# Kernel optimization log

Hardware: AMD Instinct MI355X
Metric: run time of the kernel (lower is better)

The kernel has to match this reference:

```python
import jax, jax.numpy as jnp
import numpy as np

N_NODES = 100000
N_EDGES = 3200000
N_FEAT = 128
HIDDEN = 16


def gcn_conv(x, W, b, row, col, ew, n):
    """PyG GCNConv: linear -> add self-loops -> sym deg-norm -> scatter-add -> bias."""
    x = x @ W  # [n, out]
    loop = jnp.arange(n)
    row = jnp.concatenate([row, loop])
    col = jnp.concatenate([col, loop])
    ew = jnp.concatenate([ew, jnp.ones((n,), ew.dtype)])  # self-loop weight 1
    deg = jax.ops.segment_sum(ew, col, num_segments=n)  # in-degree by edge weight
    dinv = jnp.where(deg > 0, jax.lax.rsqrt(deg), 0.0)
    norm = dinv[row] * ew * dinv[col]  # [E+n]
    # gather source features, scale, scatter-add at destinations
    out = jax.ops.segment_sum(x[row] * norm[:, None], col, num_segments=n)
    return out + b


def setup_inputs() -> dict:
    key = jax.random.key(0)
    k = jax.random.split(key, 7)
    x = jax.random.normal(k[0], (N_NODES, N_FEAT), dtype=jnp.float32)
    edge_index = jax.random.randint(k[1], (2, N_EDGES), 0, N_NODES, dtype=jnp.int64)
    edge_weight = jax.random.uniform(k[2], (N_EDGES,), dtype=jnp.float32)
    s1 = 1.0 / np.sqrt(N_FEAT)
    s2 = 1.0 / np.sqrt(HIDDEN)
    W1 = jax.random.uniform(k[3], (N_FEAT, HIDDEN), jnp.float32, -s1, s1)
    b1 = jnp.zeros((HIDDEN,), jnp.float32)
    W2 = jax.random.uniform(k[4], (HIDDEN, 1), jnp.float32, -s2, s2)
    b2 = jnp.zeros((1,), jnp.float32)
    return {"x": x, "edge_index": edge_index, "edge_weight": edge_weight,
            "W1": W1, "b1": b1, "W2": W2, "b2": b2}


def reference(x, edge_index, edge_weight, W1, b1, W2, b2):
    n = x.shape[0]
    row, col = edge_index[0], edge_index[1]
    h = gcn_conv(x, W1, b1, row, col, edge_weight, n)
    h = jax.nn.relu(h)
    h = gcn_conv(h, W2, b2, row, col, edge_weight, n)
    return jax.nn.sigmoid(h)[:, 0].astype(jnp.float32)  # squeeze(1)
```

## Files before the change

### kernel.cpp

```cpp
#include <hip/hip_runtime.h>
#include <hip/hip_fp16.h>
#include <math.h>

#define NNODES 100000
#define NEDGES 3200000
#define NF 128
#define NH 16
#define SB 192
#define NSB 521
#define NBLK 512
#define EPB (NEDGES / NBLK)
#define CAP2 6912
#define XWBLK 391

__device__ __forceinline__ __half2 u2h(unsigned u) { union { unsigned u; __half2 h; } c; c.u = u; return c.h; }
__device__ __forceinline__ unsigned h2u(__half2 h) { union { unsigned u; __half2 h; } c; c.h = h; return c.u; }
__device__ __forceinline__ __half2 shfl_h2(__half2 v, int m) {
    int x = __shfl_xor(*(int*)&v, m);
    return *(__half2*)&x;
}

__global__ void k_histxw(const int* __restrict__ col, unsigned* __restrict__ ghist,
                         const float* __restrict__ x, const float* __restrict__ W1,
                         float* __restrict__ xw) {
    __shared__ float w[NF * NH];
    __shared__ unsigned h[NSB];
    int t = threadIdx.x, b = blockIdx.x;
    if (b < NBLK) {
        for (int i = t; i < NSB; i += 256) h[i] = 0u;
        __syncthreads();
        const int2* c2 = (const int2*)(col + b * EPB);
        for (int i = t; i < EPB / 2; i += 256) {
            int2 c = c2[i];
            atomicAdd(&h[(unsigned)c.x / SB], 1u);
            atomicAdd(&h[(unsigned)c.y / SB], 1u);
        }
        __syncthreads();
        for (int i = t; i < NSB; i += 256) ghist[(size_t)b * NSB + i] = h[i];
    } else {
        for (int i = t; i < NF * NH; i += 256) w[i] = W1[i];
        __syncthreads();
        int i = (b - NBLK) * 256 + t;
        if (i >= NNODES) return;
        float acc[NH];
#pragma unroll
        for (int f = 0; f < NH; ++f) acc[f] = 0.f;
        const float4* xr = (const float4*)(x + (long long)i * NF);
#pragma unroll 8
        for (int k4 = 0; k4 < NF / 4; ++k4) {
            float4 v = xr[k4];
            const float* wk = &w[k4 * 4 * NH];
#pragma unroll
            for (int f = 0; f < NH; ++f)
                acc[f] += v.x * wk[f] + v.y * wk[NH + f] + v.z * wk[2 * NH + f] + v.w * wk[3 * NH + f];
        }
        float4* o = (float4*)(xw + (size_t)i * NH);
#pragma unroll
        for (int q = 0; q < 4; ++q)
            o[q] = make_float4(acc[4 * q], acc[4 * q + 1], acc[4 * q + 2], acc[4 * q + 3]);
    }
}

__global__ __launch_bounds__(NBLK) void k_scan1(unsigned* __restrict__ ghist,
                                                unsigned* __restrict__ totals) {
    int k = blockIdx.x, t = threadIdx.x;
    __shared__ unsigned s[NBLK];
    unsigned v = ghist[(size_t)t * NSB + k];
    s[t] = v;
    __syncthreads();
    for (int off = 1; off < NBLK; off <<= 1) {
        unsigned x = (t >= off) ? s[t - off] : 0u;
        __syncthreads();
        s[t] += x;
        __syncthreads();
    }
    ghist[(size_t)t * NSB + k] = s[t] - v;
    if (t == NBLK - 1) totals[k] = s[t];
}

__global__ void k_scan2(const unsigned* __restrict__ totals, unsigned* __restrict__ sbase,
                        unsigned* __restrict__ start) {
    int t = threadIdx.x;
    __shared__ unsigned s[256];
    unsigned v[3];
    unsigned p = 0;
#pragma unroll
    for (int j = 0; j < 3; ++j) {
        int i = t * 3 + j;
        v[j] = (i < NSB) ? totals[i] : 0u;
        p += v[j];
    }
    s[t] = p;
    __syncthreads();
    for (int off = 1; off < 256; off <<= 1) {
        unsigned x = (t >= off) ? s[t - off] : 0u;
        __syncthreads();
        s[t] += x;
        __syncthreads();
    }
    unsigned run = s[t] - p;
#pragma unroll
    for (int j = 0; j < 3; ++j) {
        int i = t * 3 + j;
        if (i < NSB) sbase[i] = run;
        run += v[j];
    }
    if (t == 255) { sbase[NSB] = NEDGES; start[NNODES] = NEDGES; }
}

__global__ __launch_bounds__(256) void k_scatB1(
        const int* __restrict__ row, const int* __restrict__ col,
        const float* __restrict__ ew,
        const unsigned* __restrict__ ghist, const unsigned* __restrict__ sbase,
        uint2* __restrict__ spack) {
    __shared__ uint2 stage[EPB];
    __shared__ unsigned short sbArr[EPB];
    __shared__ unsigned lcnt[NSB];
    __shared__ unsigned gdelta[NSB];
    __shared__ unsigned scn[256];
    int t = threadIdx.x, b = blockIdx.x;
    int e0 = b * EPB;
    for (int i = t; i < NSB; i += 256) lcnt[i] = 0u;
    __syncthreads();
    const int2* c2 = (const int2*)(col + e0);
    for (int i = t; i < EPB / 2; i += 256) {
        int2 c = c2[i];
        atomicAdd(&lcnt[(unsigned)c.x / SB], 1u);
        atomicAdd(&lcnt[(unsigned)c.y / SB], 1u);
    }
    __syncthreads();
    unsigned v[3];
    unsigned p = 0;
#pragma unroll
    for (int j = 0; j < 3; ++j) {
        int i = t * 3 + j;
        v[j] = (i < NSB) ? lcnt[i] : 0u;
        p += v[j];
    }
    scn[t] = p;
    __syncthreads();
    for (int off = 1; off < 256; off <<= 1) {
        unsigned x = (t >= off) ? scn[t - off] : 0u;
        __syncthreads();
        scn[t] += x;
        __syncthreads();
    }
    unsigned run = scn[t] - p;
    __syncthreads();
    unsigned lst[3];
#pragma unroll
    for (int j = 0; j < 3; ++j) {
        int i = t * 3 + j;
        if (i < NSB) {
            lst[j] = run;
            gdelta[i] = sbase[i] + ghist[(size_t)b * NSB + i] - run;
        }
        run += v[j];
    }
    __syncthreads();
#pragma unroll
    for (int j = 0; j < 3; ++j) {
        int i = t * 3 + j;
        if (i < NSB) lcnt[i] = lst[j];
    }
    __syncthreads();
    const int2* r2 = (const int2*)(row + e0);
    const float2* w2 = (const float2*)(ew + e0);
    for (int i = t; i < EPB / 2; i += 256) {
        int2 rr = r2[i];
        int2 cc = c2[i];
        float2 ww = w2[i];
        unsigned sb = (unsigned)cc.x / SB;
        unsigned ln = (unsigned)cc.x - sb * SB;
        unsigned pos = atomicAdd(&lcnt[sb], 1u);
        stage[pos] = make_uint2((unsigned)rr.x | (ln << 17), __float_as_uint(ww.x));
        sbArr[pos] = (unsigned short)sb;
        sb = (unsigned)cc.y / SB;
        ln = (unsigned)cc.y - sb * SB;
        pos = atomicAdd(&lcnt[sb], 1u);
        stage[pos] = make_uint2((unsigned)rr.y | (ln << 17), __float_as_uint(ww.y));
        sbArr[pos] = (unsigned short)sb;
    }
    __syncthreads();
    for (int i = t; i < EPB; i += 256)
        spack[i + gdelta[sbArr[i]]] = stage[i];
}

__global__ __launch_bounds__(512) void k_degdinv(
        const uint2* __restrict__ spack, const unsigned* __restrict__ sbase,
        unsigned* __restrict__ start, float* __restrict__ dinv,
        const float* __restrict__ xw, unsigned* __restrict__ xwn) {
    __shared__ unsigned hist[SB];
    __shared__ float wdeg[SB];
    __shared__ unsigned scn[512];
    int k = blockIdx.x, t = threadIdx.x;
    unsigned e0 = sbase[k], e1 = sbase[k + 1];
    int ne = (int)(e1 - e0);
    if (t < SB) { hist[t] = 0u; wdeg[t] = 0.f; }
    __syncthreads();
    for (int i = t; i < ne; i += 512) {
        uint2 p = spack[e0 + i];
        unsigned ln = p.x >> 17;
        atomicAdd(&hist[ln], 1u);
        atomicAdd(&wdeg[ln], __uint_as_float(p.y));
    }
    __syncthreads();
    unsigned v = (t < SB) ? hist[t] : 0u;
    scn[t] = v;
    __syncthreads();
    for (int off = 1; off < 512; off <<= 1) {
        unsigned x = (t >= off) ? scn[t - off] : 0u;
        __syncthreads();
        scn[t] += x;
        __syncthreads();
    }
    unsigned excl = scn[t] - v;
    int g = k * SB + t;
    if (t < SB && g < NNODES) {
        start[g] = e0 + excl;
        float di = rsqrtf(wdeg[t] + 1.0f);
        dinv[g] = di;
        const float4* xr = (const float4*)(xw + (size_t)g * NH);
        float4 A = xr[0], B = xr[1], C = xr[2], D = xr[3];
        uint4 o0, o1;
        o0.x = h2u(__floats2half2_rn(A.x * di, A.y * di));
        o0.y = h2u(__floats2half2_rn(A.z * di, A.w * di));
        o0.z = h2u(__floats2half2_rn(B.x * di, B.y * di));
        o0.w = h2u(__floats2half2_rn(B.z * di, B.w * di));
        o1.x = h2u(__floats2half2_rn(C.x * di, C.y * di));
        o1.y = h2u(__floats2half2_rn(C.z * di, C.w * di));
        o1.z = h2u(__floats2half2_rn(D.x * di, D.y * di));
        o1.w = h2u(__floats2half2_rn(D.z * di, D.w * di));
        uint4* o = (uint4*)(xwn + (size_t)g * 8);
        o[0] = o0;
        o[1] = o1;
    }
}

__global__ __launch_bounds__(1024) void k_sedge1(
        const uint2* __restrict__ spack, const unsigned* __restrict__ sbase,
        const unsigned* __restrict__ start, const unsigned* __restrict__ xwn,
        const float* __restrict__ dinv, const float* __restrict__ b1,
        const float* __restrict__ W2, float* __restrict__ zn) {
    __shared__ uint2 ed[CAP2];
    __shared__ unsigned lcnt[SB];
    int k = blockIdx.x, t = threadIdx.x;
    unsigned e0 = sbase[k], e1 = sbase[k + 1];
    int ne = (int)(e1 - e0);
    if (t < SB) {
        int g = k * SB + t;
        lcnt[t] = (g < NNODES) ? (start[g] - e0) : (unsigned)ne;
    }
    __syncthreads();
    for (int i = t; i < ne; i += 1024) {
        uint2 p = spack[e0 + i];
        unsigned ln = p.x >> 17;
        unsigned pos = atomicAdd(&lcnt[ln], 1u);
        __half2 hw = __float2half2_rn(__uint_as_float(p.y));
        ed[pos] = make_uint2(p.x & 0x1FFFFu, h2u(hw));
    }
    __syncthreads();
    int wave = t >> 6, lane = t & 63;
    int fg = lane & 3, e4 = lane >> 2;
#pragma unroll
    for (int j = 0; j < SB / 16; ++j) {
        int ln = wave * (SB / 16) + j;
        int g = k * SB + ln;
        if (g >= NNODES) break;
        unsigned o0 = (ln == 0) ? 0u : lcnt[ln - 1];
        unsigned o1 = lcnt[ln];
        __half2 a0 = __float2half2_rn(0.f), a1 = a0;
        for (unsigned e = o0 + e4; e < o1; e += 16) {
            uint2 d = ed[e];
            uint2 q = *(const uint2*)(xwn + (size_t)d.x * 8 + fg * 2);
            a0 = __hfma2(u2h(q.x), u2h(d.y), a0);
            a1 = __hfma2(u2h(q.y), u2h(d.y), a1);
        }
#pragma unroll
        for (int m = 4; m < 64; m <<= 1) {
            a0 = __hadd2(a0, shfl_h2(a0, m));
            a1 = __hadd2(a1, shfl_h2(a1, m));
        }
        float ax = __low2float(a0), ay = __high2float(a0);
        float az = __low2float(a1), aw = __high2float(a1);
        uint2 qs = *(const uint2*)(xwn + (size_t)g * 8 + fg * 2);
        ax += __low2float(u2h(qs.x)); ay += __high2float(u2h(qs.x));
        az += __low2float(u2h(qs.y)); aw += __high2float(u2h(qs.y));
        float di = dinv[g];
        float4 b4 = ((const float4*)b1)[fg];
        float4 w4 = ((const float4*)W2)[fg];
        float s = fmaxf(di * ax + b4.x, 0.f) * w4.x
                + fmaxf(di * ay + b4.y, 0.f) * w4.y
                + fmaxf(di * az + b4.z, 0.f) * w4.z
                + fmaxf(di * aw + b4.w, 0.f) * w4.w;
        s += __shfl_xor(s, 1);
        s += __shfl_xor(s, 2);
        if (lane == 0) zn[g] = s * di;
    }
}

__global__ __launch_bounds__(512) void k_edge2acc(
        const uint2* __restrict__ spack, const unsigned* __restrict__ sbase,
        const float* __restrict__ zn, const float* __restrict__ dinv,
        const float* __restrict__ b2, float* __restrict__ out) {
    __shared__ float zacc[SB];
    int k = blockIdx.x, t = threadIdx.x;
    if (t < SB) zacc[t] = 0.f;
    __syncthreads();
    unsigned e0 = sbase[k], e1 = sbase[k + 1];
    for (unsigned e = e0 + t; e < e1; e += 512) {
        uint2 p = spack[e];
        atomicAdd(&zacc[p.x >> 17], zn[p.x & 0x1FFFFu] * __uint_as_float(p.y));
    }
    __syncthreads();
    int g = k * SB + t;
    if (t < SB && g < NNODES) {
        float di = dinv[g];
        float v = di * zacc[t] + di * zn[g] + b2[0];
        out[g] = 1.f / (1.f + expf(-v));
    }
}

extern "C" void kernel_launch(void* const* d_in, const int* in_sizes, int n_in,
                              void* d_out, int out_size, void* d_ws, size_t ws_size,
                              hipStream_t stream) {
    const float* x  = (const float*)d_in[0];
    const int* eidx = (const int*)d_in[1];
    const float* ew = (const float*)d_in[2];
    const float* W1 = (const float*)d_in[3];
    const float* b1 = (const float*)d_in[4];
    const float* W2 = (const float*)d_in[5];
    const float* b2 = (const float*)d_in[6];
    float* out = (float*)d_out;

    const int* row = eidx;
    const int* col = eidx + NEDGES;

    unsigned* ws = (unsigned*)d_ws;
    uint2*    spack  = (uint2*)ws;
    float*    xw     = (float*)(ws + 6400000);
    unsigned* xwn    = ws + 8000000;
    float*    dinv   = (float*)(ws + 8800000);
    float*    zn     = (float*)(ws + 8900000);
    unsigned* start  = ws + 9000000;
    unsigned* sbase  = ws + 9100001;
    unsigned* totals = ws + 9100523;
    unsigned* ghist  = ws + 9101044;

    k_histxw <<<NBLK + XWBLK, 256, 0, stream>>>(col, ghist, x, W1, xw);
    k_scan1  <<<NSB, NBLK, 0, stream>>>(ghist, totals);
    k_scan2  <<<1, 256, 0, stream>>>(totals, sbase, start);
    k_scatB1 <<<NBLK, 256, 0, stream>>>(row, col, ew, ghist, sbase, spack);
    k_degdinv<<<NSB, 512, 0, stream>>>(spack, sbase, start, dinv, xw, xwn);
    k_sedge1 <<<NSB, 1024, 0, stream>>>(spack, sbase, start, xwn, dinv, b1, W2, zn);
    k_edge2acc<<<NSB, 512, 0, stream>>>(spack, sbase, zn, dinv, b2, out);
}
```

Measured before the change: 139.4 us.

## Fold superblock scan into scatter kernel and store XW in half precision

Removes the single-block k_scan2 launch by having every scatter block redundantly scan the superblock totals, with block 0 writing sbase. XW is now written directly as fp16 by the histogram/matmul kernel, and the source-side dinv scaling moves from a per-node prescale into the per-edge weight during edge staging. The scatter kernel also goes from 256 to 512 threads per block. This trades one launch and an XW fp32 round trip for a redundant scan per block and an extra dinv gather per edge, and it no longer writes start[NNODES].

```diff
diff --git a/kernel.cpp b/kernel.cpp
--- a/kernel.cpp
+++ b/kernel.cpp
@@ -22,7 +22,7 @@
 
 __global__ void k_histxw(const int* __restrict__ col, unsigned* __restrict__ ghist,
                          const float* __restrict__ x, const float* __restrict__ W1,
-                         float* __restrict__ xw) {
+                         unsigned* __restrict__ xwh) {
     __shared__ float w[NF * NH];
     __shared__ unsigned h[NSB];
     int t = threadIdx.x, b = blockIdx.x;
@@ -54,10 +54,13 @@
             for (int f = 0; f < NH; ++f)
                 acc[f] += v.x * wk[f] + v.y * wk[NH + f] + v.z * wk[2 * NH + f] + v.w * wk[3 * NH + f];
         }
-        float4* o = (float4*)(xw + (size_t)i * NH);
-#pragma unroll
-        for (int q = 0; q < 4; ++q)
-            o[q] = make_float4(acc[4 * q], acc[4 * q + 1], acc[4 * q + 2], acc[4 * q + 3]);
+        unsigned u[8];
+#pragma unroll
+        for (int j = 0; j < 8; ++j)
+            u[j] = h2u(__floats2half2_rn(acc[2 * j], acc[2 * j + 1]));
+        uint4* o = (uint4*)(xwh + (size_t)i * 8);
+        o[0] = make_uint4(u[0], u[1], u[2], u[3]);
+        o[1] = make_uint4(u[4], u[5], u[6], u[7]);
     }
 }
 
@@ -78,68 +81,59 @@
     if (t == NBLK - 1) totals[k] = s[t];
 }
 
-__global__ void k_scan2(const unsigned* __restrict__ totals, unsigned* __restrict__ sbase,
-                        unsigned* __restrict__ start) {
-    int t = threadIdx.x;
-    __shared__ unsigned s[256];
-    unsigned v[3];
-    unsigned p = 0;
-#pragma unroll
-    for (int j = 0; j < 3; ++j) {
-        int i = t * 3 + j;
-        v[j] = (i < NSB) ? totals[i] : 0u;
-        p += v[j];
-    }
-    s[t] = p;
-    __syncthreads();
-    for (int off = 1; off < 256; off <<= 1) {
-        unsigned x = (t >= off) ? s[t - off] : 0u;
-        __syncthreads();
-        s[t] += x;
-        __syncthreads();
-    }
-    unsigned run = s[t] - p;
-#pragma unroll
-    for (int j = 0; j < 3; ++j) {
-        int i = t * 3 + j;
-        if (i < NSB) sbase[i] = run;
-        run += v[j];
-    }
-    if (t == 255) { sbase[NSB] = NEDGES; start[NNODES] = NEDGES; }
-}
-
-__global__ __launch_bounds__(256) void k_scatB1(
+__global__ __launch_bounds__(512) void k_scatB1(
         const int* __restrict__ row, const int* __restrict__ col,
         const float* __restrict__ ew,
-        const unsigned* __restrict__ ghist, const unsigned* __restrict__ sbase,
-        uint2* __restrict__ spack) {
+        const unsigned* __restrict__ ghist, const unsigned* __restrict__ totals,
+        uint2* __restrict__ spack, unsigned* __restrict__ sbase_out) {
     __shared__ uint2 stage[EPB];
     __shared__ unsigned short sbArr[EPB];
     __shared__ unsigned lcnt[NSB];
     __shared__ unsigned gdelta[NSB];
-    __shared__ unsigned scn[256];
+    __shared__ unsigned scn[512];
     int t = threadIdx.x, b = blockIdx.x;
     int e0 = b * EPB;
-    for (int i = t; i < NSB; i += 256) lcnt[i] = 0u;
+    for (int i = t; i < NSB; i += 512) lcnt[i] = 0u;
     __syncthreads();
     const int2* c2 = (const int2*)(col + e0);
-    for (int i = t; i < EPB / 2; i += 256) {
+    for (int i = t; i < EPB / 2; i += 512) {
         int2 c = c2[i];
         atomicAdd(&lcnt[(unsigned)c.x / SB], 1u);
         atomicAdd(&lcnt[(unsigned)c.y / SB], 1u);
     }
     __syncthreads();
-    unsigned v[3];
+    unsigned tv[2];
+    unsigned tp = 0;
+#pragma unroll
+    for (int j = 0; j < 2; ++j) {
+        int i = t * 2 + j;
+        tv[j] = (i < NSB) ? totals[i] : 0u;
+        tp += tv[j];
+    }
+    scn[t] = tp;
+    __syncthreads();
+    for (int off = 1; off < 512; off <<= 1) {
+        unsigned x = (t >= off) ? scn[t - off] : 0u;
+        __syncthreads();
+        scn[t] += x;
+        __syncthreads();
+    }
+    unsigned trun = scn[t] - tp;
+    unsigned sb_[2];
+#pragma unroll
+    for (int j = 0; j < 2; ++j) { sb_[j] = trun; trun += tv[j]; }
+    __syncthreads();
+    unsigned v[2];
     unsigned p = 0;
 #pragma unroll
-    for (int j = 0; j < 3; ++j) {
-        int i = t * 3 + j;
+    for (int j = 0; j < 2; ++j) {
+        int i = t * 2 + j;
         v[j] = (i < NSB) ? lcnt[i] : 0u;
         p += v[j];
     }
     scn[t] = p;
     __syncthreads();
-    for (int off = 1; off < 256; off <<= 1) {
+    for (int off = 1; off < 512; off <<= 1) {
         unsigned x = (t >= off) ? scn[t - off] : 0u;
         __syncthreads();
         scn[t] += x;
@@ -147,26 +141,34 @@
     }
     unsigned run = scn[t] - p;
     __syncthreads();
-    unsigned lst[3];
-#pragma unroll
-    for (int j = 0; j < 3; ++j) {
-        int i = t * 3 + j;
+    unsigned lst[2];
+#pragma unroll
+    for (int j = 0; j < 2; ++j) {
+        int i = t * 2 + j;
         if (i < NSB) {
             lst[j] = run;
-            gdelta[i] = sbase[i] + ghist[(size_t)b * NSB + i] - run;
+            gdelta[i] = sb_[j] + ghist[(size_t)b * NSB + i] - run;
         }
         run += v[j];
     }
     __syncthreads();
 #pragma unroll
-    for (int j = 0; j < 3; ++j) {
-        int i = t * 3 + j;
+    for (int j = 0; j < 2; ++j) {
+        int i = t * 2 + j;
         if (i < NSB) lcnt[i] = lst[j];
+    }
+    if (b == 0) {
+#pragma unroll
+        for (int j = 0; j < 2; ++j) {
+            int i = t * 2 + j;
+            if (i < NSB) sbase_out[i] = sb_[j];
+        }
+        if (t == 0) sbase_out[NSB] = NEDGES;
     }
     __syncthreads();
     const int2* r2 = (const int2*)(row + e0);
     const float2* w2 = (const float2*)(ew + e0);
-    for (int i = t; i < EPB / 2; i += 256) {
+    for (int i = t; i < EPB / 2; i += 512) {
         int2 rr = r2[i];
         int2 cc = c2[i];
         float2 ww = w2[i];
@@ -182,14 +184,13 @@
         sbArr[pos] = (unsigned short)sb;
     }
     __syncthreads();
-    for (int i = t; i < EPB; i += 256)
+    for (int i = t; i < EPB; i += 512)
         spack[i + gdelta[sbArr[i]]] = stage[i];
 }
 
 __global__ __launch_bounds__(512) void k_degdinv(
         const uint2* __restrict__ spack, const unsigned* __restrict__ sbase,
-        unsigned* __restrict__ start, float* __restrict__ dinv,
-        const float* __restrict__ xw, unsigned* __restrict__ xwn) {
+        unsigned* __restrict__ start, float* __restrict__ dinv) {
     __shared__ unsigned hist[SB];
     __shared__ float wdeg[SB];
     __shared__ unsigned scn[512];
@@ -218,28 +219,13 @@
     int g = k * SB + t;
     if (t < SB && g < NNODES) {
         start[g] = e0 + excl;
-        float di = rsqrtf(wdeg[t] + 1.0f);
-        dinv[g] = di;
-        const float4* xr = (const float4*)(xw + (size_t)g * NH);
-        float4 A = xr[0], B = xr[1], C = xr[2], D = xr[3];
-        uint4 o0, o1;
-        o0.x = h2u(__floats2half2_rn(A.x * di, A.y * di));
-        o0.y = h2u(__floats2half2_rn(A.z * di, A.w * di));
-        o0.z = h2u(__floats2half2_rn(B.x * di, B.y * di));
-        o0.w = h2u(__floats2half2_rn(B.z * di, B.w * di));
-        o1.x = h2u(__floats2half2_rn(C.x * di, C.y * di));
-        o1.y = h2u(__floats2half2_rn(C.z * di, C.w * di));
-        o1.z = h2u(__floats2half2_rn(D.x * di, D.y * di));
-        o1.w = h2u(__floats2half2_rn(D.z * di, D.w * di));
-        uint4* o = (uint4*)(xwn + (size_t)g * 8);
-        o[0] = o0;
-        o[1] = o1;
+        dinv[g] = rsqrtf(wdeg[t] + 1.0f);
     }
 }
 
 __global__ __launch_bounds__(1024) void k_sedge1(
         const uint2* __restrict__ spack, const unsigned* __restrict__ sbase,
-        const unsigned* __restrict__ start, const unsigned* __restrict__ xwn,
+        const unsigned* __restrict__ start, const unsigned* __restrict__ xwh,
         const float* __restrict__ dinv, const float* __restrict__ b1,
         const float* __restrict__ W2, float* __restrict__ zn) {
     __shared__ uint2 ed[CAP2];
@@ -255,9 +241,10 @@
     for (int i = t; i < ne; i += 1024) {
         uint2 p = spack[e0 + i];
         unsigned ln = p.x >> 17;
+        unsigned r = p.x & 0x1FFFFu;
+        float wd = __uint_as_float(p.y) * dinv[r];
         unsigned pos = atomicAdd(&lcnt[ln], 1u);
-        __half2 hw = __float2half2_rn(__uint_as_float(p.y));
-        ed[pos] = make_uint2(p.x & 0x1FFFFu, h2u(hw));
+        ed[pos] = make_uint2(r, h2u(__float2half2_rn(wd)));
     }
     __syncthreads();
     int wave = t >> 6, lane = t & 63;
@@ -272,7 +259,7 @@
         __half2 a0 = __float2half2_rn(0.f), a1 = a0;
         for (unsigned e = o0 + e4; e < o1; e += 16) {
             uint2 d = ed[e];
-            uint2 q = *(const uint2*)(xwn + (size_t)d.x * 8 + fg * 2);
+            uint2 q = *(const uint2*)(xwh + (size_t)d.x * 8 + fg * 2);
             a0 = __hfma2(u2h(q.x), u2h(d.y), a0);
             a1 = __hfma2(u2h(q.y), u2h(d.y), a1);
         }
@@ -281,12 +268,12 @@
             a0 = __hadd2(a0, shfl_h2(a0, m));
             a1 = __hadd2(a1, shfl_h2(a1, m));
         }
-        float ax = __low2float(a0), ay = __high2float(a0);
-        float az = __low2float(a1), aw = __high2float(a1);
-        uint2 qs = *(const uint2*)(xwn + (size_t)g * 8 + fg * 2);
-        ax += __low2float(u2h(qs.x)); ay += __high2float(u2h(qs.x));
-        az += __low2float(u2h(qs.y)); aw += __high2float(u2h(qs.y));
         float di = dinv[g];
+        uint2 qs = *(const uint2*)(xwh + (size_t)g * 8 + fg * 2);
+        float ax = __low2float(a0)  + di * __low2float(u2h(qs.x));
+        float ay = __high2float(a0) + di * __high2float(u2h(qs.x));
+        float az = __low2float(a1)  + di * __low2float(u2h(qs.y));
+        float aw = __high2float(a1) + di * __high2float(u2h(qs.y));
         float4 b4 = ((const float4*)b1)[fg];
         float4 w4 = ((const float4*)W2)[fg];
         float s = fmaxf(di * ax + b4.x, 0.f) * w4.x
@@ -338,20 +325,18 @@
 
     unsigned* ws = (unsigned*)d_ws;
     uint2*    spack  = (uint2*)ws;
-    float*    xw     = (float*)(ws + 6400000);
-    unsigned* xwn    = ws + 8000000;
-    float*    dinv   = (float*)(ws + 8800000);
-    float*    zn     = (float*)(ws + 8900000);
-    unsigned* start  = ws + 9000000;
-    unsigned* sbase  = ws + 9100001;
-    unsigned* totals = ws + 9100523;
-    unsigned* ghist  = ws + 9101044;
-
-    k_histxw <<<NBLK + XWBLK, 256, 0, stream>>>(col, ghist, x, W1, xw);
+    unsigned* xwh    = ws + 6400000;
+    float*    dinv   = (float*)(ws + 7200000);
+    float*    zn     = (float*)(ws + 7300000);
+    unsigned* start  = ws + 7400000;
+    unsigned* sbase  = ws + 7500000;
+    unsigned* totals = ws + 7500522;
+    unsigned* ghist  = ws + 7501043;
+
+    k_histxw <<<NBLK + XWBLK, 256, 0, stream>>>(col, ghist, x, W1, xwh);
     k_scan1  <<<NSB, NBLK, 0, stream>>>(ghist, totals);
-    k_scan2  <<<1, 256, 0, stream>>>(totals, sbase, start);
-    k_scatB1 <<<NBLK, 256, 0, stream>>>(row, col, ew, ghist, sbase, spack);
-    k_degdinv<<<NSB, 512, 0, stream>>>(spack, sbase, start, dinv, xw, xwn);
-    k_sedge1 <<<NSB, 1024, 0, stream>>>(spack, sbase, start, xwn, dinv, b1, W2, zn);
+    k_scatB1 <<<NBLK, 512, 0, stream>>>(row, col, ew, ghist, totals, spack, sbase);
+    k_degdinv<<<NSB, 512, 0, stream>>>(spack, sbase, start, dinv);
+    k_sedge1 <<<NSB, 1024, 0, stream>>>(spack, sbase, start, xwh, dinv, b1, W2, zn);
     k_edge2acc<<<NSB, 512, 0, stream>>>(spack, sbase, zn, dinv, b2, out);
 }
```

Result: slower. 145.9 us (+4.7%).
